# Kernel tuning notes

Measured on AMD Instinct MI355X. Metric: run time of the kernel, lower is better.

The kernel has to match this reference:

```python
import jax, jax.numpy as jnp
import numpy as np
import itertools

DIM = 9  # LUT resolution per axis
B, C, H, W = 4, 5, 1024, 1024


def setup_inputs() -> dict:
    key = jax.random.key(0)
    k1, k2 = jax.random.split(key)
    x = jax.random.uniform(k1, (B, C, H, W), dtype=jnp.float32)  # pixel values in [0,1]
    LUT = jax.random.normal(k2, (1, 5, DIM, DIM, DIM, DIM, DIM), dtype=jnp.float32)
    return {"x": x, "LUT": LUT}


def _pglut_transform(x, LUT):
    # x: [B,5,H,W] in [0,1]; LUT: [1,5,dim,dim,dim,dim,dim]
    dim = LUT.shape[2]
    scale = jnp.float32(dim - 1)
    xs = x * scale                                   # [B,5,H,W]
    idx = jnp.clip(jnp.floor(xs), 0, dim - 2).astype(jnp.int32)
    frac = xs - idx.astype(x.dtype)                  # [B,5,H,W], in [0,1]

    lut_flat = LUT[0].reshape(5, dim ** 5)           # [5, dim^5]
    # flattened base index of the lower corner of the hypercube: [B,H,W]
    base = sum(idx[:, d] * int(dim ** (4 - d)) for d in range(5))

    out = jnp.zeros((5,) + base.shape, x.dtype)      # [5,B,H,W]
    for corner in itertools.product((0, 1), repeat=5):
        offset = sum(c * int(dim ** (4 - d)) for d, c in enumerate(corner))
        # quinlinear weight: prod_d (frac_d if corner else 1-frac_d)
        w = jnp.ones(base.shape, x.dtype)
        for d, c in enumerate(corner):
            w = w * (frac[:, d] if c else (1.0 - frac[:, d]))
        vals = lut_flat[:, base + offset]            # gather -> [5,B,H,W]
        out = out + w[None] * vals
    return jnp.transpose(out, (1, 0, 2, 3))          # [B,5,H,W]


def reference(x, LUT):
    return _pglut_transform(x, LUT)
```

## Files before the change

### kernel.cpp

```cpp
#include <hip/hip_runtime.h>
#include <hip/hip_fp16.h>


#define HW_    (1024 * 1024)
#define NPIX   (4 * HW_)
#define LUTC   59049
#define NBIN   512
#define CAP    8704
#define OVFCAP 65536
#define PXB    4096
#define NCELL2 (9 * 9 * 8 * 8 * 8)
#define OVF_IDX 1023

#define R_BYTES   ((size_t)NCELL2 * 80)
#define PAY_ENT   ((size_t)NBIN * CAP + OVFCAP)
#define PAY_BYTES (PAY_ENT * 16)
#define POS_BYTES ((size_t)NPIX * 4)
#define OFF_R    ((size_t)0)
#define OFF_PAY  (OFF_R + R_BYTES)
#define OFF_POS  (OFF_PAY + PAY_BYTES)
#define OFF_CNT  (OFF_POS + POS_BYTES)
#define CNT_BYTES ((size_t)4096)
#define WS_NEED  (OFF_CNT + CNT_BYTES)

typedef _Float16 v2h __attribute__((ext_vector_type(2)));
typedef float    f4v __attribute__((ext_vector_type(4)));
union H2U { __half2 h; uint u; v2h v; };
union H8U { uint4 q; __half2 h2[4]; };
union HQ8 { __half h[8]; uint4 q; };

__global__ __launch_bounds__(256) void k1_buildR(
    const float* __restrict__ lut, __half* __restrict__ R)
{
    __shared__ float s[5 * 162];
    int bid = blockIdx.x;
    int i2 = bid & 7;
    int r  = bid >> 3;
    int Q  = r * 9 + i2;
    const int fb = Q * 81;
    for (int u = threadIdx.x; u < 5 * 162; u += 256) {
        int c = u / 162; int j = u - c * 162;
        s[u] = lut[(size_t)c * LUTC + fb + j];
    }
    __syncthreads();
    int cellBaseG = bid * 64;
    for (int t = threadIdx.x; t < 320; t += 256) {
        int cell = t / 5; int c = t - cell * 5;
        int i3 = cell >> 3, i4 = cell & 7;
        const float* L = s + c * 162 + i3 * 9 + i4;
        HQ8 u;
        u.h[0] = __float2half(L[0]);   u.h[1] = __float2half(L[81]);
        u.h[2] = __float2half(L[1]);   u.h[3] = __float2half(L[82]);
        u.h[4] = __float2half(L[9]);   u.h[5] = __float2half(L[90]);
        u.h[6] = __float2half(L[10]);  u.h[7] = __float2half(L[91]);
        ((uint4*)R)[(size_t)(cellBaseG + cell) * 5 + c] = u.q;
    }
}

__global__ __launch_bounds__(1024) void k4_fused(
    const float* __restrict__ x,
    uint* __restrict__ gcnt,
    uint4* __restrict__ pay, uint* __restrict__ sortpos)
{
    __shared__ uint4  sPay[PXB];
    __shared__ uint   sStart[NBIN];
    __shared__ uint   sCur[NBIN];
    __shared__ uint   sCB[NBIN];
    __shared__ uint   sWsum[8];

    int tid = threadIdx.x, blk = blockIdx.x;
    if (tid < NBIN) sCur[tid] = 0;
    __syncthreads();

    int pBase = blk * PXB + tid * 4;
    int b = pBase >> 20, hw = pBase & (HW_ - 1);
    const float* xp = x + (size_t)b * 5 * HW_ + hw;
    f4v xv[5];
    #pragma unroll
    for (int d = 0; d < 5; ++d)
        xv[d] = __builtin_nontemporal_load((const f4v*)(xp + (size_t)d * HW_));

    uint4 plr[4]; uint keyr[4];
    #pragma unroll
    for (int j = 0; j < 4; ++j) {
        float f[5]; int idx[5];
        #pragma unroll
        for (int d = 0; d < 5; ++d) {
            float xs = xv[d][j] * 8.0f;
            int i = (int)floorf(xs); i = i < 0 ? 0 : (i > 7 ? 7 : i);
            idx[d] = i; f[d] = xs - (float)i;
        }
        int key   = (idx[0] << 6) | (idx[1] << 3) | idx[2];
        int local = (idx[3] << 3) | idx[4];
        H2U a, bq, c;
        a.h  = __float22half2_rn(make_float2(f[0], f[1]));
        bq.h = __float22half2_rn(make_float2(f[2], f[3]));
        c.h  = __float22half2_rn(make_float2(f[4], 0.f));
        plr[j].x = a.u; plr[j].y = bq.u; plr[j].z = c.u;
        plr[j].w = (uint)(pBase + j) | ((uint)local << 22);
        keyr[j] = (uint)key;
        atomicAdd(&sCur[key], 1u);
    }
    __syncthreads();

    uint v = 0, s = 0, base = 0;
    if (tid < NBIN) {
        v = sCur[tid];
        if (v) base = atomicAdd(&gcnt[tid * 2], v);
        s = v;
        #pragma unroll
        for (int off = 1; off < 64; off <<= 1) {
            uint t = __shfl_up(s, off);
            if ((tid & 63) >= off) s += t;
        }
        if ((tid & 63) == 63) sWsum[tid >> 6] = s;
    }
    __syncthreads();
    if (tid < NBIN) {
        uint add = 0;
        #pragma unroll
        for (int w = 0; w < 8; ++w)
            add += (w < (tid >> 6)) ? sWsum[w] : 0u;
        sStart[tid] = s + add - v;
        sCB[tid]    = base;
        sCur[tid]   = 0;
    }
    __syncthreads();

    uint dstr[4];
    #pragma unroll
    for (int j = 0; j < 4; ++j) {
        uint key  = keyr[j];
        uint rank = atomicAdd(&sCur[key], 1u);
        uint slot = sStart[key] + rank;
        sPay[slot] = plr[j];
        uint gIdx = sCB[key] + rank;
        uint dst;
        if (gIdx < CAP) {
            dst = key * CAP + gIdx;
        } else {
            uint oi = atomicAdd(&gcnt[OVF_IDX], 1u);
            if (oi >= OVFCAP) oi = OVFCAP - 1;
            pay[(size_t)NBIN * CAP + oi] = plr[j];
            dst = (uint)(NBIN * CAP) + oi;
        }
        dstr[j] = dst;
    }
    *(uint4*)(sortpos + pBase) = make_uint4(dstr[0], dstr[1], dstr[2], dstr[3]);
    __syncthreads();

    {
        int wave = tid >> 6, lane = tid & 63;
        uint wbase = (uint)wave * 32;
        #pragma unroll
        for (int g = 0; g < 4; ++g) {
            uint bin = wbase + g * 8 + (lane >> 3);
            uint cnt = sCur[bin];
            uint st  = sStart[bin];
            uint cb  = sCB[bin];
            uint4* gp = pay + (size_t)bin * CAP;
            for (uint e = (uint)(lane & 7); e < cnt; e += 8) {
                uint gIdx = cb + e;
                if (gIdx < CAP)
                    gp[gIdx] = sPay[st + e];
            }
        }
    }
}

__global__ __launch_bounds__(256) void k5_compute(
    const __half* __restrict__ R, const uint* __restrict__ gcnt,
    uint4* __restrict__ pay)
{
    __shared__ uint4 stbl[1280];
    int bid = blockIdx.x;
    int bin = bid >> 2, q = bid & 3;
    int i0 = bin >> 6, i1 = (bin >> 3) & 7, i2 = bin & 7;
    const uint4* R4 = (const uint4*)R;
    #pragma unroll
    for (int slab = 0; slab < 4; ++slab) {
        int a = slab >> 1, bcorner = slab & 1;
        size_t srcBase = (size_t)((((i0 + a) * 9 + (i1 + bcorner)) * 8 + i2) * 64) * 5;
        for (int rr = threadIdx.x; rr < 320; rr += 256)
            stbl[slab * 320 + rr] = R4[srcBase + rr];
    }
    __syncthreads();
    uint n = gcnt[bin * 2]; if (n > CAP) n = CAP;
    uint B0 = (uint)bin * CAP;
    uint st = B0 + ((n * q) >> 2), en = B0 + ((n * (q + 1)) >> 2);
    for (uint i = st + threadIdx.x; i < en; i += 256) {
        uint4 pl = pay[i];
        H2U f01, f23, f4x; f01.u = pl.x; f23.u = pl.y; f4x.u = pl.z;
        float2 F01 = __half22float2(f01.h);
        float2 F23 = __half22float2(f23.h);
        float f0 = F01.x, f1 = F01.y, f2 = F23.x;
        __half2 f33 = __half2half2(__high2half(f23.h));
        __half2 f44 = __half2half2(__low2half(f4x.h));
        int local = (int)(pl.w >> 22);
        const uint4* cbase = stbl + local * 5;
        float g0 = 1.f - f0, g1 = 1.f - f1, g2 = 1.f - f2;
        H2U wv[4];
        float w00 = g0 * g1, w01c = g0 * f1, w10 = f0 * g1, w11 = f0 * f1;
        wv[0].h = __float22half2_rn(make_float2(w00  * g2, w00  * f2));
        wv[1].h = __float22half2_rn(make_float2(w01c * g2, w01c * f2));
        wv[2].h = __float22half2_rn(make_float2(w10  * g2, w10  * f2));
        wv[3].h = __float22half2_rn(make_float2(w11  * g2, w11  * f2));
        float acc[5];
        #pragma unroll
        for (int c = 0; c < 5; ++c) acc[c] = 0.f;
        #pragma unroll
        for (int slab = 0; slab < 4; ++slab) {
            #pragma unroll
            for (int c = 0; c < 5; ++c) {
                H8U u; u.q = cbase[slab * 320 + c];
                __half2 e0 = __hfma2(f44, __hsub2(u.h2[1], u.h2[0]), u.h2[0]);
                __half2 e1 = __hfma2(f44, __hsub2(u.h2[3], u.h2[2]), u.h2[2]);
                H2U dd; dd.h = __hfma2(f33, __hsub2(e1, e0), e0);
#if __has_builtin(__builtin_amdgcn_fdot2)
                acc[c] = __builtin_amdgcn_fdot2(dd.v, wv[slab].v, acc[c], false);
#else
                float2 D = __half22float2(dd.h);
                float2 W = __half22float2(wv[slab].h);
                acc[c] = fmaf(D.x, W.x, fmaf(D.y, W.y, acc[c]));
#endif
            }
        }
        H2U o01, o23, o4x;
        o01.h = __float22half2_rn(make_float2(acc[0], acc[1]));
        o23.h = __float22half2_rn(make_float2(acc[2], acc[3]));
        o4x.h = __float22half2_rn(make_float2(acc[4], 0.f));
        uint4 res; res.x = o01.u; res.y = o23.u; res.z = o4x.u; res.w = pl.w;
        pay[i] = res;
    }
}

__global__ __launch_bounds__(256) void k5_ovf(
    const float* __restrict__ x, const __half* __restrict__ R,
    const uint* __restrict__ gcnt, uint4* __restrict__ pay)
{
    uint n = gcnt[OVF_IDX]; if (n > OVFCAP) n = OVFCAP;
    for (uint i = blockIdx.x * 256 + threadIdx.x; i < n; i += 64 * 256) {
        uint4 pl = pay[(size_t)NBIN * CAP + i];
        uint p = pl.w & 0x3FFFFFu;
        int b = p >> 20, hw = p & (HW_ - 1);
        const float* xp = x + (size_t)b * 5 * HW_ + hw;
        float f[5]; int idx[5];
        #pragma unroll
        for (int d = 0; d < 5; ++d) {
            float xs = xp[(size_t)d * HW_] * 8.0f;
            int ii = (int)floorf(xs); ii = ii < 0 ? 0 : (ii > 7 ? 7 : ii);
            idx[d] = ii; f[d] = xs - (float)ii;
        }
        float g0 = 1.f - f[0], g1 = 1.f - f[1];
        float f2 = f[2], f3 = f[3], f4 = f[4];
        int cellBase = ((idx[0] * 9 + idx[1]) * 8 + idx[2]) * 64 + idx[3] * 8 + idx[4];
        float acc[5];
        #pragma unroll
        for (int c = 0; c < 5; ++c) acc[c] = 0.f;
        #pragma unroll
        for (int c0 = 0; c0 < 2; ++c0) {
            float w0 = c0 ? f[0] : g0;
            int o0 = cellBase + c0 * 4608;
            #pragma unroll
            for (int c1 = 0; c1 < 2; ++c1) {
                float w = w0 * (c1 ? f[1] : g1);
                const uint4* pc = (const uint4*)R + (size_t)(o0 + c1 * 512) * 5;
                #pragma unroll
                for (int c = 0; c < 5; ++c) {
                    HQ8 u; u.q = pc[c];
                    float e00 = __half2float(u.h[0]) + f2 * (__half2float(u.h[1]) - __half2float(u.h[0]));
                    float e01 = __half2float(u.h[2]) + f2 * (__half2float(u.h[3]) - __half2float(u.h[2]));
                    float e10 = __half2float(u.h[4]) + f2 * (__half2float(u.h[5]) - __half2float(u.h[4]));
                    float e11 = __half2float(u.h[6]) + f2 * (__half2float(u.h[7]) - __half2float(u.h[6]));
                    float d0 = e00 + f4 * (e01 - e00);
                    float d1 = e10 + f4 * (e11 - e10);
                    float vv = d0 + f3 * (d1 - d0);
                    acc[c] = fmaf(w, vv, acc[c]);
                }
            }
        }
        H2U o01, o23, o4x;
        o01.h = __float22half2_rn(make_float2(acc[0], acc[1]));
        o23.h = __float22half2_rn(make_float2(acc[2], acc[3]));
        o4x.h = __float22half2_rn(make_float2(acc[4], 0.f));
        uint4 res; res.x = o01.u; res.y = o23.u; res.z = o4x.u; res.w = pl.w;
        pay[(size_t)NBIN * CAP + i] = res;
    }
}

__global__ __launch_bounds__(1024) void k6_unpermute(
    const uint* __restrict__ sortpos, const uint4* __restrict__ res,
    float* __restrict__ out)
{
    int pBase = blockIdx.x * 4096 + threadIdx.x * 4;
    uint4 d4 = *(const uint4*)(sortpos + pBase);
    uint4 r0 = res[d4.x];
    uint4 r1 = res[d4.y];
    uint4 r2 = res[d4.z];
    uint4 r3 = res[d4.w];
    H2U a0, a1, a2, a3, b0, b1, b2, b3, c0, c1, c2, c3;
    a0.u = r0.x; b0.u = r0.y; c0.u = r0.z;
    a1.u = r1.x; b1.u = r1.y; c1.u = r1.z;
    a2.u = r2.x; b2.u = r2.y; c2.u = r2.z;
    a3.u = r3.x; b3.u = r3.y; c3.u = r3.z;
    float2 A0 = __half22float2(a0.h), A1 = __half22float2(a1.h);
    float2 A2 = __half22float2(a2.h), A3 = __half22float2(a3.h);
    float2 B0 = __half22float2(b0.h), B1 = __half22float2(b1.h);
    float2 B2 = __half22float2(b2.h), B3 = __half22float2(b3.h);
    float2 C0 = __half22float2(c0.h), C1 = __half22float2(c1.h);
    float2 C2 = __half22float2(c2.h), C3 = __half22float2(c3.h);
    int b = pBase >> 20, hw = pBase & (HW_ - 1);
    float* op = out + (size_t)b * 5 * HW_ + hw;
    f4v o;
    o[0] = A0.x; o[1] = A1.x; o[2] = A2.x; o[3] = A3.x;
    __builtin_nontemporal_store(o, (f4v*)(op));
    o[0] = A0.y; o[1] = A1.y; o[2] = A2.y; o[3] = A3.y;
    __builtin_nontemporal_store(o, (f4v*)(op + HW_));
    o[0] = B0.x; o[1] = B1.x; o[2] = B2.x; o[3] = B3.x;
    __builtin_nontemporal_store(o, (f4v*)(op + 2 * HW_));
    o[0] = B0.y; o[1] = B1.y; o[2] = B2.y; o[3] = B3.y;
    __builtin_nontemporal_store(o, (f4v*)(op + 3 * HW_));
    o[0] = C0.x; o[1] = C1.x; o[2] = C2.x; o[3] = C3.x;
    __builtin_nontemporal_store(o, (f4v*)(op + 4 * HW_));
}

__global__ __launch_bounds__(256) void buildR3(
    const float* __restrict__ lut, __half* __restrict__ R)
{
    int t = blockIdx.x * blockDim.x + threadIdx.x;
    if (t >= 5 * NCELL2) return;
    int cell = t / 5;
    int c    = t - cell * 5;
    int i4 = cell & 7;
    int i3 = (cell >> 3) & 7;
    int i2 = (cell >> 6) & 7;
    int r  = cell >> 9;
    int i1 = r % 9;
    int i0 = r / 9;
    int flat = (((i0 * 9 + i1) * 9 + i2) * 9 + i3) * 9 + i4;
    const float* qq = lut + c * LUTC + flat;
    HQ8 u;
    u.h[0] = __float2half(qq[0]);  u.h[1] = __float2half(qq[1]);
    u.h[2] = __float2half(qq[9]);  u.h[3] = __float2half(qq[10]);
    u.h[4] = __float2half(qq[81]); u.h[5] = __float2half(qq[82]);
    u.h[6] = __float2half(qq[90]); u.h[7] = __float2half(qq[91]);
    ((uint4*)R)[t] = u.q;
}

__device__ __forceinline__ float lerpf(float a, float b, float t) {
    return fmaf(t, b - a, a);
}

__global__ __launch_bounds__(256) void gather3(
    const float* __restrict__ x, const __half* __restrict__ R,
    float* __restrict__ out)
{
    int p = blockIdx.x * blockDim.x + threadIdx.x;
    if (p >= NPIX) return;
    int b  = p >> 20;
    int hw = p & (HW_ - 1);
    const float* xp = x + (size_t)b * 5 * HW_ + hw;
    float f[5], g[5]; int idx[5];
    #pragma unroll
    for (int d = 0; d < 5; ++d) {
        float xs = __builtin_nontemporal_load(xp + (size_t)d * HW_) * 8.0f;
        int i = (int)floorf(xs); i = i < 0 ? 0 : (i > 7 ? 7 : i);
        idx[d] = i; f[d] = xs - (float)i; g[d] = 1.0f - f[d];
    }
    const float f2 = f[2], f3 = f[3], f4 = f[4];
    int base = ((idx[0] * 9 + idx[1]) * 8 + idx[2]) * 64 + idx[3] * 8 + idx[4];
    float acc0 = 0.f, acc1 = 0.f, acc2 = 0.f, acc3 = 0.f, acc4 = 0.f;
    #pragma unroll
    for (int c0 = 0; c0 < 2; ++c0) {
        const float w0 = c0 ? f[0] : g[0];
        const int  o0  = base + c0 * 4608;
        #pragma unroll
        for (int c1 = 0; c1 < 2; ++c1) {
            const float w  = w0 * (c1 ? f[1] : g[1]);
            const __half* pc = R + (size_t)(o0 + c1 * 512) * 40;
            #pragma unroll
            for (int c = 0; c < 5; ++c) {
                HQ8 u; u.q = *(const uint4*)(pc + c * 8);
                float v000 = __half2float(u.h[0]);
                float v001 = __half2float(u.h[1]);
                float v010 = __half2float(u.h[2]);
                float v011 = __half2float(u.h[3]);
                float v100 = __half2float(u.h[4]);
                float v101 = __half2float(u.h[5]);
                float v110 = __half2float(u.h[6]);
                float v111 = __half2float(u.h[7]);
                float e00 = lerpf(v000, v001, f2);
                float e01 = lerpf(v010, v011, f2);
                float e10 = lerpf(v100, v101, f2);
                float e11 = lerpf(v110, v111, f2);
                float d0  = lerpf(e00, e01, f4);
                float d1  = lerpf(e10, e11, f4);
                float s   = lerpf(d0, d1, f3);
                if      (c == 0) acc0 = fmaf(w, s, acc0);
                else if (c == 1) acc1 = fmaf(w, s, acc1);
                else if (c == 2) acc2 = fmaf(w, s, acc2);
                else if (c == 3) acc3 = fmaf(w, s, acc3);
                else             acc4 = fmaf(w, s, acc4);
            }
        }
    }
    float* op = out + (size_t)b * 5 * HW_ + hw;
    __builtin_nontemporal_store(acc0, op + 0 * HW_);
    __builtin_nontemporal_store(acc1, op + 1 * HW_);
    __builtin_nontemporal_store(acc2, op + 2 * HW_);
    __builtin_nontemporal_store(acc3, op + 3 * HW_);
    __builtin_nontemporal_store(acc4, op + 4 * HW_);
}

extern "C" void kernel_launch(void* const* d_in, const int* in_sizes, int n_in,
                              void* d_out, int out_size, void* d_ws, size_t ws_size,
                              hipStream_t stream)
{
    const float* x   = (const float*)d_in[0];
    const float* lut = (const float*)d_in[1];
    float* out       = (float*)d_out;
    char* ws         = (char*)d_ws;

    if (ws != nullptr && ws_size >= WS_NEED) {
        __half* R      = (__half*)(ws + OFF_R);
        uint4*  pay    = (uint4*)(ws + OFF_PAY);
        uint*   sortp  = (uint*)(ws + OFF_POS);
        uint*   gcnt   = (uint*)(ws + OFF_CNT);

        hipMemsetAsync(gcnt, 0, CNT_BYTES, stream);
        k1_buildR   <<<648, 256, 0, stream>>>(lut, R);
        k4_fused    <<<NPIX / PXB, 1024, 0, stream>>>(x, gcnt, pay, sortp);
        k5_compute  <<<4 * NBIN, 256, 0, stream>>>(R, gcnt, pay);
        k5_ovf      <<<64, 256, 0, stream>>>(x, R, gcnt, pay);
        k6_unpermute<<<NPIX / 4096, 1024, 0, stream>>>(sortp, pay, out);
    } else if (ws != nullptr && ws_size >= R_BYTES) {
        __half* R = (__half*)ws;
        int nb = (5 * NCELL2 + 255) / 256;
        buildR3<<<nb, 256, 0, stream>>>(lut, R);
        gather3<<<NPIX / 256, 256, 0, stream>>>(x, R, out);
    }
}
```

Before: 241.0 us.

## Sort bin entries by local cell in shared memory before LUT interpolation

Each quarter-bin chunk is split into two halves of up to 1152 entries. Each half is counting-sorted by the 6-bit local cell index using a shared histogram, a wave prefix scan and atomic scatter. Entries are then processed in sorted order and results are written back to their original positions through a permutation array. The aim is to reduce LDS bank conflicts and divergence when threads read the shared LUT slabs. The cost is extra barriers, shared atomics and scattered global writes. Chunks larger than 1280 entries would overflow the per-thread registers, so correctness depends on bin occupancy staying within that limit.

```diff
diff --git a/kernel.cpp b/kernel.cpp
--- a/kernel.cpp
+++ b/kernel.cpp
@@ -168,11 +168,64 @@
     }
 }
 
+__device__ __forceinline__ uint4 k5_entry(
+    const uint4* __restrict__ stbl, uint4 pl)
+{
+    H2U f01, f23, f4x; f01.u = pl.x; f23.u = pl.y; f4x.u = pl.z;
+    float2 F01 = __half22float2(f01.h);
+    float2 F23 = __half22float2(f23.h);
+    float f0 = F01.x, f1 = F01.y, f2 = F23.x;
+    __half2 f33 = __half2half2(__high2half(f23.h));
+    __half2 f44 = __half2half2(__low2half(f4x.h));
+    int local = (int)(pl.w >> 22);
+    const uint4* cbase = stbl + local * 5;
+    float g0 = 1.f - f0, g1 = 1.f - f1, g2 = 1.f - f2;
+    H2U wv[4];
+    float w00 = g0 * g1, w01c = g0 * f1, w10 = f0 * g1, w11 = f0 * f1;
+    wv[0].h = __float22half2_rn(make_float2(w00  * g2, w00  * f2));
+    wv[1].h = __float22half2_rn(make_float2(w01c * g2, w01c * f2));
+    wv[2].h = __float22half2_rn(make_float2(w10  * g2, w10  * f2));
+    wv[3].h = __float22half2_rn(make_float2(w11  * g2, w11  * f2));
+    float acc[5];
+    #pragma unroll
+    for (int c = 0; c < 5; ++c) acc[c] = 0.f;
+    #pragma unroll
+    for (int slab = 0; slab < 4; ++slab) {
+        #pragma unroll
+        for (int c = 0; c < 5; ++c) {
+            H8U u; u.q = cbase[slab * 320 + c];
+            __half2 e0 = __hfma2(f44, __hsub2(u.h2[1], u.h2[0]), u.h2[0]);
+            __half2 e1 = __hfma2(f44, __hsub2(u.h2[3], u.h2[2]), u.h2[2]);
+            H2U dd; dd.h = __hfma2(f33, __hsub2(e1, e0), e0);
+#if __has_builtin(__builtin_amdgcn_fdot2)
+            acc[c] = __builtin_amdgcn_fdot2(dd.v, wv[slab].v, acc[c], false);
+#else
+            float2 D = __half22float2(dd.h);
+            float2 W = __half22float2(wv[slab].h);
+            acc[c] = fmaf(D.x, W.x, fmaf(D.y, W.y, acc[c]));
+#endif
+        }
+    }
+    H2U o01, o23, o4x;
+    o01.h = __float22half2_rn(make_float2(acc[0], acc[1]));
+    o23.h = __float22half2_rn(make_float2(acc[2], acc[3]));
+    o4x.h = __float22half2_rn(make_float2(acc[4], 0.f));
+    uint4 res; res.x = o01.u; res.y = o23.u; res.z = o4x.u; res.w = pl.w;
+    return res;
+}
+
 __global__ __launch_bounds__(256) void k5_compute(
     const __half* __restrict__ R, const uint* __restrict__ gcnt,
     uint4* __restrict__ pay)
 {
-    __shared__ uint4 stbl[1280];
+    __shared__ uint4  stbl[1280];
+    __shared__ uint4  sEnt[1152];
+    __shared__ ushort sPerm[1152];
+    __shared__ uint   sLH[64];
+    __shared__ uint   sLS[64];
+    __shared__ uint   sLC[64];
+
+    int tid = threadIdx.x;
     int bid = blockIdx.x;
     int bin = bid >> 2, q = bid & 3;
     int i0 = bin >> 6, i1 = (bin >> 3) & 7, i2 = bin & 7;
@@ -181,56 +234,53 @@
     for (int slab = 0; slab < 4; ++slab) {
         int a = slab >> 1, bcorner = slab & 1;
         size_t srcBase = (size_t)((((i0 + a) * 9 + (i1 + bcorner)) * 8 + i2) * 64) * 5;
-        for (int rr = threadIdx.x; rr < 320; rr += 256)
+        for (int rr = tid; rr < 320; rr += 256)
             stbl[slab * 320 + rr] = R4[srcBase + rr];
     }
-    __syncthreads();
     uint n = gcnt[bin * 2]; if (n > CAP) n = CAP;
     uint B0 = (uint)bin * CAP;
-    uint st = B0 + ((n * q) >> 2), en = B0 + ((n * (q + 1)) >> 2);
-    for (uint i = st + threadIdx.x; i < en; i += 256) {
-        uint4 pl = pay[i];
-        H2U f01, f23, f4x; f01.u = pl.x; f23.u = pl.y; f4x.u = pl.z;
-        float2 F01 = __half22float2(f01.h);
-        float2 F23 = __half22float2(f23.h);
-        float f0 = F01.x, f1 = F01.y, f2 = F23.x;
-        __half2 f33 = __half2half2(__high2half(f23.h));
-        __half2 f44 = __half2half2(__low2half(f4x.h));
-        int local = (int)(pl.w >> 22);
-        const uint4* cbase = stbl + local * 5;
-        float g0 = 1.f - f0, g1 = 1.f - f1, g2 = 1.f - f2;
-        H2U wv[4];
-        float w00 = g0 * g1, w01c = g0 * f1, w10 = f0 * g1, w11 = f0 * f1;
-        wv[0].h = __float22half2_rn(make_float2(w00  * g2, w00  * f2));
-        wv[1].h = __float22half2_rn(make_float2(w01c * g2, w01c * f2));
-        wv[2].h = __float22half2_rn(make_float2(w10  * g2, w10  * f2));
-        wv[3].h = __float22half2_rn(make_float2(w11  * g2, w11  * f2));
-        float acc[5];
-        #pragma unroll
-        for (int c = 0; c < 5; ++c) acc[c] = 0.f;
-        #pragma unroll
-        for (int slab = 0; slab < 4; ++slab) {
+    uint qs = (n * (uint)q) >> 2, qe = (n * (uint)(q + 1)) >> 2;
+
+    for (int h = 0; h < 2; ++h) {
+        uint cs = qs + (((qe - qs) * (uint)h) >> 1);
+        uint ce = qs + (((qe - qs) * (uint)(h + 1)) >> 1);
+        uint cn = ce - cs;
+        __syncthreads();
+        if (tid < 64) sLH[tid] = 0;
+        __syncthreads();
+
+        uint4 e0, e1, e2, e3, e4;
+        uint k0 = (uint)tid, k1 = k0 + 256, k2 = k0 + 512, k3 = k0 + 768, k4 = k0 + 1024;
+        if (k0 < cn) { e0 = pay[B0 + cs + k0]; atomicAdd(&sLH[e0.w >> 22], 1u); }
+        if (k1 < cn) { e1 = pay[B0 + cs + k1]; atomicAdd(&sLH[e1.w >> 22], 1u); }
+        if (k2 < cn) { e2 = pay[B0 + cs + k2]; atomicAdd(&sLH[e2.w >> 22], 1u); }
+        if (k3 < cn) { e3 = pay[B0 + cs + k3]; atomicAdd(&sLH[e3.w >> 22], 1u); }
+        if (k4 < cn) { e4 = pay[B0 + cs + k4]; atomicAdd(&sLH[e4.w >> 22], 1u); }
+        __syncthreads();
+
+        if (tid < 64) {
+            uint v = sLH[tid], s = v;
             #pragma unroll
-            for (int c = 0; c < 5; ++c) {
-                H8U u; u.q = cbase[slab * 320 + c];
-                __half2 e0 = __hfma2(f44, __hsub2(u.h2[1], u.h2[0]), u.h2[0]);
-                __half2 e1 = __hfma2(f44, __hsub2(u.h2[3], u.h2[2]), u.h2[2]);
-                H2U dd; dd.h = __hfma2(f33, __hsub2(e1, e0), e0);
-#if __has_builtin(__builtin_amdgcn_fdot2)
-                acc[c] = __builtin_amdgcn_fdot2(dd.v, wv[slab].v, acc[c], false);
-#else
-                float2 D = __half22float2(dd.h);
-                float2 W = __half22float2(wv[slab].h);
-                acc[c] = fmaf(D.x, W.x, fmaf(D.y, W.y, acc[c]));
-#endif
+            for (int off = 1; off < 64; off <<= 1) {
+                uint t = __shfl_up(s, off);
+                if (tid >= off) s += t;
             }
-        }
-        H2U o01, o23, o4x;
-        o01.h = __float22half2_rn(make_float2(acc[0], acc[1]));
-        o23.h = __float22half2_rn(make_float2(acc[2], acc[3]));
-        o4x.h = __float22half2_rn(make_float2(acc[4], 0.f));
-        uint4 res; res.x = o01.u; res.y = o23.u; res.z = o4x.u; res.w = pl.w;
-        pay[i] = res;
+            sLS[tid] = s - v;
+            sLC[tid] = 0;
+        }
+        __syncthreads();
+
+        if (k0 < cn) { uint l = e0.w >> 22; uint p = sLS[l] + atomicAdd(&sLC[l], 1u); sEnt[p] = e0; sPerm[p] = (ushort)k0; }
+        if (k1 < cn) { uint l = e1.w >> 22; uint p = sLS[l] + atomicAdd(&sLC[l], 1u); sEnt[p] = e1; sPerm[p] = (ushort)k1; }
+        if (k2 < cn) { uint l = e2.w >> 22; uint p = sLS[l] + atomicAdd(&sLC[l], 1u); sEnt[p] = e2; sPerm[p] = (ushort)k2; }
+        if (k3 < cn) { uint l = e3.w >> 22; uint p = sLS[l] + atomicAdd(&sLC[l], 1u); sEnt[p] = e3; sPerm[p] = (ushort)k3; }
+        if (k4 < cn) { uint l = e4.w >> 22; uint p = sLS[l] + atomicAdd(&sLC[l], 1u); sEnt[p] = e4; sPerm[p] = (ushort)k4; }
+        __syncthreads();
+
+        for (uint p = tid; p < cn; p += 256) {
+            uint4 res = k5_entry(stbl, sEnt[p]);
+            pay[B0 + cs + (uint)sPerm[p]] = res;
+        }
     }
 }
 
```

Result: slower. 294.7 us (+22.3%).
